# Optimization experiments

Hardware: AMD Instinct MI355X
Metric: run time of the kernel (lower is better)

The kernel has to match this reference:

```python
import jax, jax.numpy as jnp
import numpy as np

N, E, B = 30000, 100000, 1024
FXD, FXT, D, H, NOUT = 78, 954, 128, 10, 2


def setup_inputs() -> dict:
    key = jax.random.key(0)
    ks = jax.random.split(key, 24)
    rn = lambda i, shape, s=0.05: jax.random.normal(ks[i], shape, dtype=jnp.float32) * s
    z = lambda shape: jnp.zeros(shape, dtype=jnp.float32)
    batch = ((jnp.arange(N) * B) // N).astype(jnp.int32)  # sorted, every graph id present
    return {
        "x1": rn(0, (N, FXD), 1.0),
        "edge_index1": jax.random.randint(ks[1], (2, E), 0, N, dtype=jnp.int32),
        "batch1": batch,
        "x2": rn(2, (N, FXD), 1.0),
        "edge_index2": jax.random.randint(ks[3], (2, E), 0, N, dtype=jnp.int32),
        "batch2": batch,
        "cell": jax.random.uniform(ks[4], (B, FXT), dtype=jnp.float32),
        "W1": rn(5, (FXD, H * D)), "a_src1": rn(6, (1, H, D)), "a_dst1": rn(7, (1, H, D)), "b1": z((H * D,)),
        # GATConv2: 1280 -> 128, 1 head
        "W2": rn(8, (H * D, D)), "a_src2": rn(9, (1, 1, D)), "a_dst2": rn(10, (1, 1, D)), "b2": z((D,)),
        "Wg": rn(11, (D, D)), "bg": z((D,)),
        "Wr1": rn(12, (FXT, 2048)), "br1": z((2048,)),
        "Wr2": rn(13, (2048, 512)), "br2": z((512,)),
        "Wr3": rn(14, (512, 2 * D)), "br3": z((2 * D,)),
        "Wf1": rn(15, (4 * D, 1024)), "bf1": z((1024,)),
        "Wf2": rn(16, (1024, 512)), "bf2": z((512,)),
        "Wf3": rn(17, (512, 128)), "bf3": z((128,)),
        "Wo": rn(18, (128, NOUT)), "bo": z((NOUT,)),
    }


def gat_conv(x, src, dst, W, a_src, a_dst, bias, heads, ch):
    """PyG GATConv (v1), self-loops already included in src/dst. Concat heads."""
    n = x.shape[0]
    h = (x @ W).reshape(n, heads, ch)                      # [N,H,C]
    alpha_s = jnp.sum(h * a_src, axis=-1)                  # [N,H]
    alpha_d = jnp.sum(h * a_dst, axis=-1)                  # [N,H]
    e = jax.nn.leaky_relu(alpha_s[src] + alpha_d[dst], 0.2)  # [E',H]
    emax = jax.ops.segment_max(e, dst, num_segments=n)     # segment softmax over dst
    ex = jnp.exp(e - emax[dst])
    denom = jax.ops.segment_sum(ex, dst, num_segments=n)
    alpha = ex / (denom[dst] + 1e-16)                      # [E',H]
    msg = h[src] * alpha[:, :, None]                       # [E',H,C]
    out = jax.ops.segment_sum(msg, dst, num_segments=n)    # [N,H,C]
    return out.reshape(n, heads * ch) + bias


def _l2norm(x):
    return x / jnp.maximum(jnp.linalg.norm(x, axis=1, keepdims=True), 1e-12)


def reference(x1, edge_index1, batch1, x2, edge_index2, batch2, cell,
              W1, a_src1, a_dst1, b1, W2, a_src2, a_dst2, b2, Wg, bg,
              Wr1, br1, Wr2, br2, Wr3, br3, Wf1, bf1, Wf2, bf2, Wf3, bf3, Wo, bo):
    def branch(x, ei, batch):
        n = x.shape[0]
        loops = jnp.arange(n, dtype=ei.dtype)              # add_self_loops=True
        src = jnp.concatenate([ei[0], loops])
        dst = jnp.concatenate([ei[1], loops])
        h = jax.nn.elu(gat_conv(x, src, dst, W1, a_src1, a_dst1, b1, H, D))
        h = jax.nn.elu(gat_conv(h, src, dst, W2, a_src2, a_dst2, b2, 1, D))
        g = jax.ops.segment_max(h, batch, num_segments=B)  # global_max_pool
        return jax.nn.relu(g @ Wg + bg)

    v1 = branch(x1, edge_index1, batch1)
    v2 = branch(x2, edge_index2, batch2)
    c = _l2norm(cell)
    c = jax.nn.relu(c @ Wr1 + br1)
    c = jax.nn.relu(c @ Wr2 + br2)
    c = jax.nn.relu(c @ Wr3 + br3)
    xc = _l2norm(jnp.concatenate([v1, v2, c], axis=1))
    xc = jax.nn.relu(xc @ Wf1 + bf1)
    xc = jax.nn.relu(xc @ Wf2 + bf2)
    xc = jax.nn.relu(xc @ Wf3 + bf3)
    return xc @ Wo + bo
```

## Files before the change

### kernel.cpp

```cpp
#include <hip/hip_runtime.h>
#include <math.h>

typedef unsigned short ushort_t;
typedef __attribute__((ext_vector_type(8))) short short8;
typedef __attribute__((ext_vector_type(8))) unsigned short ushort8v;
typedef __attribute__((ext_vector_type(4))) float float4v;
typedef __attribute__((ext_vector_type(4))) unsigned short ushort4v;

#define MPAD 30016
#define H1STR 136

__device__ __forceinline__ float lrelu02(float v){ return v > 0.f ? v : 0.2f*v; }
__device__ __forceinline__ float elu_fast(float v){ return v > 0.f ? v : (__expf(v) - 1.f); }

__device__ __forceinline__ ushort_t f2bf(float x){
  unsigned u = __float_as_uint(x);
  return (ushort_t)((u + 0x7fffu + ((u >> 16) & 1u)) >> 16);
}
__device__ __forceinline__ float bf2f(ushort_t h){ return __uint_as_float(((unsigned)h) << 16); }

__device__ __forceinline__ unsigned encf(float f){
  unsigned u = __float_as_uint(f);
  return (u & 0x80000000u) ? ~u : (u | 0x80000000u);
}
__device__ __forceinline__ float decf(unsigned u){
  return __uint_as_float((u >> 31) ? (u & 0x7FFFFFFFu) : ~u);
}

__device__ __forceinline__ void gll16(const void* g, void* l){
  __builtin_amdgcn_global_load_lds((const __attribute__((address_space(1))) void*)g,
                                   (__attribute__((address_space(3))) void*)l, 16, 0, 0);
}

__global__ void hist2_k(const int* __restrict__ ei1, const int* __restrict__ ei2,
                        int E, int N, int* deg){
  int idx = blockIdx.x*blockDim.x + threadIdx.x;
  if (idx < 2*E){
    int br = idx / E, e = idx - br*E;
    const int* ei = br ? ei2 : ei1;
    atomicAdd(&deg[br*N + ei[E + e]], 1);
  }
}

__global__ __launch_bounds__(1024)
void scanA_k(const int* __restrict__ deg, int* __restrict__ rowptr, int* __restrict__ bsum, int n){
  int br = blockIdx.y;
  int t = threadIdx.x;
  int i = blockIdx.x*1024 + t;
  __shared__ int s[1024];
  int v = (i < n) ? (deg[br*n + i] + 1) : 0;
  s[t] = v; __syncthreads();
  for (int off = 1; off < 1024; off <<= 1){
    int x = (t >= off) ? s[t - off] : 0;
    __syncthreads();
    s[t] += x;
    __syncthreads();
  }
  if (i < n) rowptr[br*(n+1) + i] = s[t] - v;
  if (t == 1023) bsum[br*gridDim.x + blockIdx.x] = s[1023];
}

__global__ void scanB_k(int* bsum, int nb){
  int br = threadIdx.x;
  if (br < 2){
    int run = 0;
    for (int i = 0; i < nb; ++i){ int v = bsum[br*nb + i]; bsum[br*nb + i] = run; run += v; }
  }
}

__global__ __launch_bounds__(1024)
void scanC_k(const int* __restrict__ bsum, int* __restrict__ rowptr, int* __restrict__ cursor,
             int n, int nb, int total){
  int br = blockIdx.y;
  int i = blockIdx.x*1024 + threadIdx.x;
  int add = bsum[br*nb + blockIdx.x];
  if (i < n){
    int nv = rowptr[br*(n+1) + i] + add;
    rowptr[br*(n+1) + i] = nv;
    cursor[br*n + i] = nv;
  }
  if (i == 0) rowptr[br*(n+1) + n] = total;
}

__global__ void fill_csr2_k(const int* __restrict__ ei1, const int* __restrict__ ei2,
                            int E, int N, int* cursor, int* csr){
  int idx = blockIdx.x*blockDim.x + threadIdx.x;
  if (idx < 2*E){
    int br = idx / E, e = idx - br*E;
    const int* ei = br ? ei2 : ei1;
    int dst = ei[E + e];
    int pos = atomicAdd(&cursor[br*N + dst], 1);
    csr[br*(E+N) + pos] = ei[e];
  } else if (idx < 2*E + 2*N){
    int r = idx - 2*E;
    int br = r / N, i = r - br*N;
    int pos = atomicAdd(&cursor[br*N + i], 1);
    csr[br*(E+N) + pos] = i;
  }
}

__global__ void mkattn_k(const float* __restrict__ W1, const float* __restrict__ a_src1,
                         const float* __restrict__ a_dst1,
                         const float* __restrict__ W2, const float* __restrict__ a_src2,
                         const float* __restrict__ a_dst2,
                         float* As, float* Ad, float* vs, float* vd){
  int idx = blockIdx.x*blockDim.x + threadIdx.x;
  if (idx < 780){
    int f = idx / 10, h = idx % 10;
    float ss = 0.f, sd = 0.f;
    for (int c = 0; c < 128; ++c){
      float w = W1[f*1280 + h*128 + c];
      ss += w * a_src1[h*128 + c];
      sd += w * a_dst1[h*128 + c];
    }
    As[idx] = ss; Ad[idx] = sd;
  } else if (idx < 2060){
    int k = idx - 780;
    float ss = 0.f, sd = 0.f;
    for (int c = 0; c < 128; ++c){
      float w = W2[k*128 + c];
      ss += w * a_src2[c]; sd += w * a_dst2[c];
    }
    vs[k] = ss; vd[k] = sd;
  }
}

__global__ __launch_bounds__(256)
void alpha1b_k(const float* __restrict__ x1, const float* __restrict__ x2,
               const float* __restrict__ As, const float* __restrict__ Ad,
               float* as1, float* ad1, int n){
  __shared__ float sAs[780], sAd[780];
  int t = threadIdx.x;
  for (int k = t; k < 780; k += 256){ sAs[k] = As[k]; sAd[k] = Ad[k]; }
  __syncthreads();
  int idx = blockIdx.x*256 + t;
  if (idx >= 2*n) return;
  int br = idx / n, i = idx - br*n;
  const float* xr = (br ? x2 : x1) + (size_t)i*78;
  float ss[10], sd[10];
  #pragma unroll
  for (int h = 0; h < 10; ++h){ ss[h] = 0.f; sd[h] = 0.f; }
  for (int f = 0; f < 78; ++f){
    float xv = xr[f];
    #pragma unroll
    for (int h = 0; h < 10; ++h){
      ss[h] += xv * sAs[f*10 + h];
      sd[h] += xv * sAd[f*10 + h];
    }
  }
  #pragma unroll
  for (int h = 0; h < 10; ++h){
    as1[(size_t)idx*10 + h] = ss[h];
    ad1[(size_t)idx*10 + h] = sd[h];
  }
}

__global__ __launch_bounds__(64)
void gat1_agg_k(const int* __restrict__ rowptr2, const int* __restrict__ csr2,
                const float* __restrict__ x1, const float* __restrict__ x2,
                const float* __restrict__ as1b, const float* __restrict__ ad1b,
                ushort_t* __restrict__ yh, int n, int E){
  int gi = blockIdx.x;
  int br = (gi >= n) ? 1 : 0;
  int i = gi - br*n;
  int t = threadIdx.x;
  const int* rowptr = rowptr2 + (size_t)br*(n+1);
  const int* csr    = csr2 + (size_t)br*(E+n);
  const float* x    = br ? x2 : x1;
  const float* as1  = as1b + (size_t)br*n*10;
  ushort_t* yb      = yh + (size_t)br*10*MPAD*96;

  __shared__ float adi[10], rden[10], wE[10], xs[78];
  int beg = rowptr[i], end = rowptr[i+1];
  if (t < 10) adi[t] = ad1b[(size_t)gi*10 + t];
  __syncthreads();
  float den = 0.f;
  float acc[13];
  int hh[13], cc[13];
  #pragma unroll
  for (int k = 0; k < 13; ++k){
    acc[k] = 0.f;
    int j = t + 64*k;
    hh[k] = (j < 780) ? (j/78) : 0;
    cc[k] = (j < 780) ? (j%78) : 0;
  }
  for (int e = beg; e < end; ++e){
    int s = csr[e];
    if (t < 10){
      float w = __expf(lrelu02(as1[(size_t)s*10 + t] + adi[t]));
      wE[t] = w; den += w;
    }
    for (int c = t; c < 78; c += 64) xs[c] = x[(size_t)s*78 + c];
    __syncthreads();
    #pragma unroll
    for (int k = 0; k < 13; ++k){
      int j = t + 64*k;
      if (j < 780) acc[k] += wE[hh[k]] * xs[cc[k]];
    }
    __syncthreads();
  }
  if (t < 10) rden[t] = 1.f/(den + 1e-16f);
  __syncthreads();
  #pragma unroll
  for (int k = 0; k < 13; ++k){
    int j = t + 64*k;
    if (j < 780) yb[((size_t)hh[k]*MPAD + i)*96 + cc[k]] = f2bf(acc[k]*rden[hh[k]]);
  }
  for (int p = t; p < 180; p += 64){
    int h = p/18, c = 78 + p%18;
    yb[((size_t)h*MPAD + i)*96 + c] = 0;
  }
}

__global__ __launch_bounds__(256)
void branch_conv_k(const ushort_t* __restrict__ yall,
                   const ushort_t* __restrict__ W1h, const ushort_t* __restrict__ W2h,
                   const float* __restrict__ b1, const float* __restrict__ vs,
                   const float* __restrict__ vd,
                   ushort_t* __restrict__ h2all, float* __restrict__ as2all,
                   float* __restrict__ ad2all, int M){
  const int NBLK = MPAD/64;
  int br = blockIdx.x / NBLK;
  int bi = blockIdx.x - br*NBLK;
  const ushort_t* y = yall + (size_t)br*10*MPAD*96;
  ushort_t* h2 = h2all + (size_t)br*MPAD*128;
  float* as2 = as2all + (size_t)br*MPAD;
  float* ad2 = ad2all + (size_t)br*MPAD;

  __shared__ ushort_t stage[2][6144];
  __shared__ ushort_t h1t[64*H1STR];
  __shared__ float red[256];

  int tid = threadIdx.x, lane = tid & 63, wave = tid >> 6;
  int row0 = bi*64;
  int wm = (wave & 1)*32, wn = (wave >> 1)*64;
  int lr = lane & 15, quad = lane >> 4;
  int sr = lane >> 2;
  int skc = (((lane & 3) ^ ((lane >> 3) & 3)) * 8);
  int qs  = (quad ^ ((lr >> 1) & 3)) * 8;

  float4v acc2[2][4];
  #pragma unroll
  for (int i = 0; i < 2; ++i)
    #pragma unroll
    for (int j = 0; j < 4; ++j)
      acc2[i][j] = (float4v){0.f, 0.f, 0.f, 0.f};
  float rps[8], rpd[8];
  #pragma unroll
  for (int z = 0; z < 8; ++z){ rps[z] = 0.f; rpd[z] = 0.f; }

  for (int h = 0; h < 10; ++h){
    const ushort_t* gA   = y   + ((size_t)h*MPAD + row0 + wave*16 + sr)*96 + skc;
    const ushort_t* gB0h = W1h + ((size_t)(h*128 + wave*32      + sr))*96 + skc;
    const ushort_t* gB1h = W1h + ((size_t)(h*128 + wave*32 + 16 + sr))*96 + skc;
    const ushort_t* gC0h = W2h + ((size_t)(wave*32      + sr))*1280 + h*128 + skc;
    const ushort_t* gC1h = W2h + ((size_t)(wave*32 + 16 + sr))*1280 + h*128 + skc;

    auto issue1 = [&](int p, int kt){
      ushort_t* st = &stage[p][0];
      gll16(gA   + kt, st + wave*512);
      gll16(gB0h + kt, st + 2048 + wave*1024);
      gll16(gB1h + kt, st + 2048 + wave*1024 + 512);
    };
    auto issue2 = [&](int p, int kt){
      ushort_t* st = &stage[p][0];
      gll16(gC0h + kt, st + 2048 + wave*1024);
      gll16(gC1h + kt, st + 2048 + wave*1024 + 512);
    };

    __syncthreads();
    issue1(0, 0);
    float4v acc1[2][4];
    #pragma unroll
    for (int i = 0; i < 2; ++i)
      #pragma unroll
      for (int j = 0; j < 4; ++j)
        acc1[i][j] = (float4v){0.f, 0.f, 0.f, 0.f};
    int p = 0;
    #pragma unroll
    for (int it = 0; it < 3; ++it){
      __syncthreads();
      if (it < 2) issue1(p ^ 1, (it + 1)*32);
      const ushort_t* sm = &stage[p][0];
      short8 af[2], bhf[4];
      #pragma unroll
      for (int t2 = 0; t2 < 2; ++t2)
        af[t2] = *(const short8*)&sm[(wm + t2*16 + lr)*32 + qs];
      #pragma unroll
      for (int j = 0; j < 4; ++j)
        bhf[j] = *(const short8*)&sm[2048 + (wn + j*16 + lr)*32 + qs];
      #pragma unroll
      for (int i = 0; i < 2; ++i)
        #pragma unroll
        for (int j = 0; j < 4; ++j)
          acc1[i][j] = __builtin_amdgcn_mfma_f32_16x16x32_bf16(af[i], bhf[j], acc1[i][j], 0, 0, 0);
      p ^= 1;
    }

    #pragma unroll
    for (int j = 0; j < 4; ++j){
      int col = wn + j*16 + lr;
      float bv  = b1[h*128 + col];
      float vsv = vs[h*128 + col];
      float vdv = vd[h*128 + col];
      #pragma unroll
      for (int i = 0; i < 2; ++i){
        #pragma unroll
        for (int r = 0; r < 4; ++r){
          float v = elu_fast(acc1[i][j][r] + bv);
          h1t[(wm + i*16 + quad*4 + r)*H1STR + col] = f2bf(v);
          rps[i*4 + r] += v * vsv;
          rpd[i*4 + r] += v * vdv;
        }
      }
    }
    __syncthreads();

    issue2(0, 0);
    p = 0;
    #pragma unroll
    for (int it = 0; it < 4; ++it){
      __syncthreads();
      if (it < 3) issue2(p ^ 1, (it + 1)*32);
      const ushort_t* sm = &stage[p][0];
      int kt = it*32;
      short8 af[2], bhf[4];
      #pragma unroll
      for (int t2 = 0; t2 < 2; ++t2)
        af[t2] = *(const short8*)&h1t[(wm + t2*16 + lr)*H1STR + kt + quad*8];
      #pragma unroll
      for (int j = 0; j < 4; ++j)
        bhf[j] = *(const short8*)&sm[2048 + (wn + j*16 + lr)*32 + qs];
      #pragma unroll
      for (int i = 0; i < 2; ++i)
        #pragma unroll
        for (int j = 0; j < 4; ++j)
          acc2[i][j] = __builtin_amdgcn_mfma_f32_16x16x32_bf16(af[i], bhf[j], acc2[i][j], 0, 0, 0);
      p ^= 1;
    }
  }

  #pragma unroll
  for (int j = 0; j < 4; ++j){
    int col = wn + j*16 + lr;
    #pragma unroll
    for (int i = 0; i < 2; ++i){
      #pragma unroll
      for (int r = 0; r < 4; ++r){
        int row = row0 + wm + i*16 + quad*4 + r;
        if (row < M) h2[(size_t)row*128 + col] = f2bf(acc2[i][j][r]);
      }
    }
  }
  __syncthreads();
  #pragma unroll
  for (int z = 0; z < 8; ++z){
    float a = rps[z], d = rpd[z];
    #pragma unroll
    for (int mk = 1; mk <= 8; mk <<= 1){
      a += __shfl_xor(a, mk);
      d += __shfl_xor(d, mk);
    }
    if (lr == 0){
      int i = z >> 2, r = z & 3;
      int row = wm + i*16 + quad*4 + r;
      red[row*2 + (wave >> 1)] = a;
      red[128 + row*2 + (wave >> 1)] = d;
    }
  }
  __syncthreads();
  if (tid < 64){
    int grow = row0 + tid;
    if (grow < M){
      as2[grow] = red[tid*2] + red[tid*2 + 1];
      ad2[grow] = red[128 + tid*2] + red[128 + tid*2 + 1];
    }
  }
}

__global__ __launch_bounds__(64)
void gat2_agg_k(const int* __restrict__ rowptr2, const int* __restrict__ csr2,
                const ushort_t* __restrict__ h2all, const float* __restrict__ as2all,
                const float* __restrict__ ad2all, const float* __restrict__ b2,
                const int* __restrict__ batch1, const int* __restrict__ batch2,
                unsigned* __restrict__ poolKey, int n, int E, int Bg){
  int gi = blockIdx.x;
  int br = (gi >= n) ? 1 : 0;
  int i = gi - br*n;
  int t = threadIdx.x;
  const int* rowptr = rowptr2 + (size_t)br*(n+1);
  const int* csr    = csr2 + (size_t)br*(E+n);
  const ushort_t* h2 = h2all + (size_t)br*MPAD*128;
  const float* as2  = as2all + (size_t)br*MPAD;
  float adi = ad2all[(size_t)br*MPAD + i];
  int beg = rowptr[i], end = rowptr[i+1];
  float den = 0.f, a0 = 0.f, a1 = 0.f;
  for (int e = beg; e < end; ++e){
    int s = csr[e];
    float w = __expf(lrelu02(as2[s] + adi));
    den += w;
    unsigned u = *(const unsigned*)&h2[(size_t)s*128 + 2*t];
    a0 += w * bf2f((ushort_t)(u & 0xffffu));
    a1 += w * bf2f((ushort_t)(u >> 16));
  }
  float r = 1.f/(den + 1e-16f);
  float o0 = elu_fast(a0*r + b2[2*t]);
  float o1 = elu_fast(a1*r + b2[2*t + 1]);
  int g = (br ? batch2 : batch1)[i];
  unsigned* pk = poolKey + ((size_t)br*Bg + g)*128;
  atomicMax(&pk[2*t], encf(o0));
  atomicMax(&pk[2*t + 1], encf(o1));
}

__global__ void pool_decode_k(const unsigned* __restrict__ key,
                              ushort_t* __restrict__ ph, ushort_t* __restrict__ pl, int n){
  int i = blockIdx.x*blockDim.x + threadIdx.x;
  if (i < n){
    float v = decf(key[i]);
    ushort_t h = f2bf(v);
    ph[i] = h; pl[i] = f2bf(v - bf2f(h));
  }
}

__global__ __launch_bounds__(256)
void l2norm_split_k(const float* __restrict__ in, int cols, int Kp,
                    ushort_t* __restrict__ oh, ushort_t* __restrict__ ol){
  int r = blockIdx.x, t = threadIdx.x;
  __shared__ float s[256];
  __shared__ float scaleS;
  const float* rp = in + (size_t)r*cols;
  float p = 0.f;
  for (int k = t; k < cols; k += 256){ float v = rp[k]; p += v*v; }
  s[t] = p; __syncthreads();
  for (int o = 128; o > 0; o >>= 1){
    if (t < o) s[t] += s[t+o];
    __syncthreads();
  }
  if (t == 0) scaleS = 1.f / fmaxf(sqrtf(s[0]), 1e-12f);
  __syncthreads();
  float sc = scaleS;
  for (int k = t; k < Kp; k += 256){
    float v = (k < cols) ? rp[k]*sc : 0.f;
    ushort_t h = f2bf(v);
    size_t o2 = (size_t)r*Kp + k;
    oh[o2] = h; ol[o2] = f2bf(v - bf2f(h));
  }
}

__global__ __launch_bounds__(256)
void catnorm_k(const float* __restrict__ vall, const float* __restrict__ c3,
               ushort_t* __restrict__ oh, ushort_t* __restrict__ ol, int Bg){
  int r = blockIdx.x, t = threadIdx.x;
  __shared__ float s[256];
  __shared__ float scaleS;
  auto val = [&](int c)->float{
    if (c < 128) return vall[(size_t)r*128 + c];
    if (c < 256) return vall[((size_t)Bg + r)*128 + (c - 128)];
    return c3[(size_t)r*256 + (c - 256)];
  };
  float v0 = val(t), v1 = val(t + 256);
  s[t] = v0*v0 + v1*v1; __syncthreads();
  for (int o = 128; o > 0; o >>= 1){
    if (t < o) s[t] += s[t+o];
    __syncthreads();
  }
  if (t == 0) scaleS = 1.f / fmaxf(sqrtf(s[0]), 1e-12f);
  __syncthreads();
  float sc = scaleS;
  float a = v0*sc, b = v1*sc;
  ushort_t ha = f2bf(a), hb = f2bf(b);
  size_t o2 = (size_t)r*512;
  oh[o2 + t] = ha;       ol[o2 + t] = f2bf(a - bf2f(ha));
  oh[o2 + 256 + t] = hb; ol[o2 + 256 + t] = f2bf(b - bf2f(hb));
}

__global__ void act_split_k(const float* __restrict__ in, ushort_t* __restrict__ oh,
                            ushort_t* __restrict__ ol, int n){
  int i = blockIdx.x*blockDim.x + threadIdx.x;
  if (i < n){
    float v = fmaxf(in[i], 0.f);
    ushort_t h = f2bf(v);
    oh[i] = h; ol[i] = f2bf(v - bf2f(h));
  }
}

__device__ __forceinline__ void split_one(const float* __restrict__ W, int ldw, int colStride,
                                          int N, int K, int Np, int Kp,
                                          ushort_t* __restrict__ dh, ushort_t* __restrict__ dl,
                                          int idx){
  int n  = idx % Np;
  int r  = idx / Np;
  int k4 = r % (Kp >> 2);
  int b  = r / (Kp >> 2);
  size_t o = ((size_t)b*Np + n)*Kp + (size_t)k4*4;
  ushort4v hv, lv;
  #pragma unroll
  for (int kk = 0; kk < 4; ++kk){
    int k = k4*4 + kk;
    float v = (n < N && k < K) ? W[(size_t)k*ldw + (size_t)b*colStride + n] : 0.f;
    ushort_t h = f2bf(v);
    hv[kk] = h; lv[kk] = f2bf(v - bf2f(h));
  }
  *(ushort4v*)&dh[o] = hv;
  if (dl) *(ushort4v*)&dl[o] = lv;
}

struct SplitTable {
  const float *W1, *W2, *Wg, *Wr1, *Wr2, *Wr3, *Wf1, *Wf2, *Wf3, *Wo;
  ushort_t *W1h,*W2h,*Wgh,*Wgl,*Wr1h,*Wr1l,*Wr2h,*Wr2l;
  ushort_t *Wr3h,*Wr3l,*Wf1h,*Wf1l,*Wf2h,*Wf2l,*Wf3h,*Wf3l,*Woh,*Wol;
};

__global__ void split_all_k(SplitTable T){
  int idx = blockIdx.x*blockDim.x + threadIdx.x;
  if      (idx <   30720) split_one(T.W1, 1280, 128, 128,   78,  128,   96, T.W1h, nullptr, idx);
  else if (idx <   71680) split_one(T.W2,  128,   0, 128, 1280,  128, 1280, T.W2h, nullptr, idx -   30720);
  else if (idx <   75776) split_one(T.Wg,  128,   0, 128,  128,  128,  128, T.Wgh, T.Wgl, idx -   71680);
  else if (idx <  567296) split_one(T.Wr1,2048,   0,2048,  954, 2048,  960, T.Wr1h,T.Wr1l,idx -   75776);
  else if (idx <  829440) split_one(T.Wr2, 512,   0, 512, 2048,  512, 2048, T.Wr2h,T.Wr2l,idx -  567296);
  else if (idx <  862208) split_one(T.Wr3, 256,   0, 256,  512,  256,  512, T.Wr3h,T.Wr3l,idx -  829440);
  else if (idx <  993280) split_one(T.Wf1,1024,   0,1024,  512, 1024,  512, T.Wf1h,T.Wf1l,idx -  862208);
  else if (idx < 1124352) split_one(T.Wf2, 512,   0, 512, 1024,  512, 1024, T.Wf2h,T.Wf2l,idx -  993280);
  else if (idx < 1140736) split_one(T.Wf3, 128,   0, 128,  512,  128,  512, T.Wf3h,T.Wf3l,idx - 1124352);
  else if (idx < 1142784) split_one(T.Wo,    2,   0,   2,  128,   64,  128, T.Woh, T.Wol, idx - 1140736);
}

__global__ __launch_bounds__(256)
void gemm_split(const ushort_t* __restrict__ Ahp, const ushort_t* __restrict__ Alp, int lda, long long sA,
                const ushort_t* __restrict__ Bhp, const ushort_t* __restrict__ Blp, int ldb, long long sB,
                float* __restrict__ C, ushort_t* __restrict__ Ch, ushort_t* __restrict__ Cl,
                int ldc, long long sC,
                const float* __restrict__ bias, int sBias,
                int M, int Nc, int K, int act, int outMode, int kSplit, int aSplit){
  int zb = blockIdx.z;
  int b = zb / kSplit, kc = zb - b*kSplit;
  Ahp += (long long)b*sA;
  Bhp += (long long)b*sB; Blp += (long long)b*sB;
  long long cOff = (long long)b*sC;
  int Kc = K / kSplit;
  int kb = kc*Kc;
  int nIter = Kc / 32;

  __shared__ ushort_t smem[18048];

  int tid = threadIdx.x, lane = tid & 63, wave = tid >> 6;
  int row0 = blockIdx.y*64, col0 = blockIdx.x*64;
  int wm = (wave & 1)*32, wn = (wave >> 1)*32;
  int lr = lane & 15, quad = lane >> 4;
  int qs = (quad ^ ((lr >> 1) & 3)) * 8;

  int srow = wave*16 + (lane >> 2);
  int skc  = (((lane & 3) ^ ((lane >> 3) & 3)) * 8);
  const ushort_t* gAh = Ahp + (long long)(row0 + srow)*lda + skc + kb;
  const ushort_t* gAl = aSplit ? (Alp + (long long)b*sA + (long long)(row0 + srow)*lda + skc + kb) : gAh;
  const ushort_t* gBh = Bhp + (long long)(col0 + srow)*ldb + skc + kb;
  const ushort_t* gBl = Blp + (long long)(col0 + srow)*ldb + skc + kb;

  float4v acc[2][2];
  #pragma unroll
  for (int i = 0; i < 2; ++i)
    #pragma unroll
    for (int j = 0; j < 2; ++j)
      acc[i][j] = (float4v){0.f, 0.f, 0.f, 0.f};

  auto issue = [&](int p, int kt){
    ushort_t* base = &smem[p*8192 + wave*512];
    gll16(gAh + kt, base);
    if (aSplit) gll16(gAl + kt, base + 2048);
    gll16(gBh + kt, base + 4096);
    gll16(gBl + kt, base + 6144);
  };

  issue(0, 0);
  int p = 0;
  for (int it = 0; it < nIter; ++it){
    __syncthreads();
    if (it + 1 < nIter) issue(p ^ 1, (it + 1)*32);
    const ushort_t* sm = &smem[p*8192];
    short8 ah[2], al[2], bh[2], bl[2];
    #pragma unroll
    for (int t2 = 0; t2 < 2; ++t2){
      int ao = (wm + t2*16 + lr)*32 + qs;
      int bo = (wn + t2*16 + lr)*32 + qs;
      ah[t2] = *(const short8*)&sm[ao];
      if (aSplit) al[t2] = *(const short8*)&sm[2048 + ao];
      bh[t2] = *(const short8*)&sm[4096 + bo];
      bl[t2] = *(const short8*)&sm[6144 + bo];
    }
    #pragma unroll
    for (int i = 0; i < 2; ++i)
      #pragma unroll
      for (int j = 0; j < 2; ++j){
        if (aSplit)
          acc[i][j] = __builtin_amdgcn_mfma_f32_16x16x32_bf16(al[i], bh[j], acc[i][j], 0, 0, 0);
        acc[i][j] = __builtin_amdgcn_mfma_f32_16x16x32_bf16(ah[i], bl[j], acc[i][j], 0, 0, 0);
        acc[i][j] = __builtin_amdgcn_mfma_f32_16x16x32_bf16(ah[i], bh[j], acc[i][j], 0, 0, 0);
      }
    p ^= 1;
  }
  __syncthreads();

  if (outMode == 0 || outMode == 2){
    #pragma unroll
    for (int j = 0; j < 2; ++j){
      int col = col0 + wn + j*16 + lr;
      if (col >= Nc) continue;
      float bv = (bias && kc == 0) ? bias[(long long)b*sBias + col] : 0.f;
      #pragma unroll
      for (int i = 0; i < 2; ++i){
        #pragma unroll
        for (int r = 0; r < 4; ++r){
          int row = row0 + wm + i*16 + quad*4 + r;
          if (row >= M) continue;
          float v = acc[i][j][r] + bv;
          if (act == 1) v = fmaxf(v, 0.f);
          else if (act == 2) v = elu_fast(v);
          long long o = cOff + (long long)row*ldc + col;
          if (outMode == 0) C[o] = v;
          else atomicAdd(&C[o], v);
        }
      }
    }
  } else {
    float* ftile = (float*)smem;
    #pragma unroll
    for (int i = 0; i < 2; ++i)
      #pragma unroll
      for (int j = 0; j < 2; ++j)
        #pragma unroll
        for (int r = 0; r < 4; ++r)
          ftile[(wm + i*16 + quad*4 + r)*68 + wn + j*16 + lr] = acc[i][j][r];
    __syncthreads();
    int row = tid >> 2, ch = (tid & 3)*16;
    int grow = row0 + row;
    if (grow < M){
      if (col0 + 64 <= Nc){
        long long o = cOff + (long long)grow*ldc + col0 + ch;
        #pragma unroll
        for (int g = 0; g < 2; ++g){
          ushort8v hv, lv;
          #pragma unroll
          for (int c = 0; c < 8; ++c){
            int cc2 = ch + g*8 + c;
            float v = ftile[row*68 + cc2];
            if (bias) v += bias[(long long)b*sBias + col0 + cc2];
            if (act == 1) v = fmaxf(v, 0.f);
            else if (act == 2) v = elu_fast(v);
            hv[c] = f2bf(v);
            lv[c] = f2bf(v - bf2f(hv[c]));
          }
          *(ushort8v*)&Ch[o + g*8] = hv;
          *(ushort8v*)&Cl[o + g*8] = lv;
        }
      } else {
        for (int c = 0; c < 16; ++c){
          int col = col0 + ch + c;
          if (col >= Nc) break;
          float v = ftile[row*68 + ch + c];
          if (bias) v += bias[(long long)b*sBias + col];
          if (act == 1) v = fmaxf(v, 0.f);
          else if (act == 2) v = elu_fast(v);
          long long o = cOff + (long long)grow*ldc + col;
          ushort_t h = f2bf(v);
          Ch[o] = h;
          Cl[o] = f2bf(v - bf2f(h));
        }
      }
    }
  }
}

extern "C" void kernel_launch(void* const* d_in, const int* in_sizes, int n_in,
                              void* d_out, int out_size, void* d_ws, size_t ws_size,
                              hipStream_t stream){
  const float* x1     = (const float*)d_in[0];
  const int*   ei1    = (const int*)  d_in[1];
  const int*   batch1 = (const int*)  d_in[2];
  const float* x2     = (const float*)d_in[3];
  const int*   ei2    = (const int*)  d_in[4];
  const int*   batch2 = (const int*)  d_in[5];
  const float* cell   = (const float*)d_in[6];
  const float* W1     = (const float*)d_in[7];
  const float* a_src1 = (const float*)d_in[8];
  const float* a_dst1 = (const float*)d_in[9];
  const float* b1     = (const float*)d_in[10];
  const float* W2     = (const float*)d_in[11];
  const float* a_src2 = (const float*)d_in[12];
  const float* a_dst2 = (const float*)d_in[13];
  const float* b2     = (const float*)d_in[14];
  const float* Wg     = (const float*)d_in[15];
  const float* bg     = (const float*)d_in[16];
  const float* Wr1    = (const float*)d_in[17];
  const float* br1    = (const float*)d_in[18];
  const float* Wr2    = (const float*)d_in[19];
  const float* br2    = (const float*)d_in[20];
  const float* Wr3    = (const float*)d_in[21];
  const float* br3    = (const float*)d_in[22];
  const float* Wf1    = (const float*)d_in[23];
  const float* bf1    = (const float*)d_in[24];
  const float* Wf2    = (const float*)d_in[25];
  const float* bf2    = (const float*)d_in[26];
  const float* Wf3    = (const float*)d_in[27];
  const float* bf3    = (const float*)d_in[28];
  const float* Wo     = (const float*)d_in[29];
  const float* bo     = (const float*)d_in[30];
  float* out = (float*)d_out;
  (void)n_in; (void)out_size; (void)ws_size;

  const int N  = in_sizes[0] / 78;
  const int E  = in_sizes[1] / 2;
  const int Bg = in_sizes[6] / 954;

  char* wsb = (char*)d_ws;
  size_t off = 0;
  auto alloc = [&](size_t bytes)->char*{
    char* p = wsb + off; off += ((bytes + 255)/256)*256; return p;
  };

  char* Yb = alloc((size_t)2*10*MPAD*96*2);
  ushort_t* yh = (ushort_t*)Yb;
  size_t yoff = 0;
  auto yalloc = [&](size_t bytes)->char*{
    char* p = Yb + yoff; yoff += ((bytes + 255)/256)*256; return p;
  };
  ushort_t* cnh  = (ushort_t*)yalloc((size_t)Bg*960*2);
  ushort_t* cnl  = (ushort_t*)yalloc((size_t)Bg*960*2);
  ushort_t* c1h  = (ushort_t*)yalloc((size_t)Bg*2048*2);
  ushort_t* c1l  = (ushort_t*)yalloc((size_t)Bg*2048*2);
  ushort_t* c2h  = (ushort_t*)yalloc((size_t)Bg*512*2);
  ushort_t* c2l  = (ushort_t*)yalloc((size_t)Bg*512*2);
  float*    c3   = (float*)   yalloc((size_t)Bg*256*4);
  ushort_t* xcnh = (ushort_t*)yalloc((size_t)Bg*512*2);
  ushort_t* xcnl = (ushort_t*)yalloc((size_t)Bg*512*2);
  ushort_t* t1h  = (ushort_t*)yalloc((size_t)Bg*1024*2);
  ushort_t* t1l  = (ushort_t*)yalloc((size_t)Bg*1024*2);
  ushort_t* t2h  = (ushort_t*)yalloc((size_t)Bg*512*2);
  ushort_t* t2l  = (ushort_t*)yalloc((size_t)Bg*512*2);
  ushort_t* t3h  = (ushort_t*)yalloc((size_t)Bg*128*2);
  ushort_t* t3l  = (ushort_t*)yalloc((size_t)Bg*128*2);
  ushort_t* pooledh = (ushort_t*)yalloc((size_t)2*Bg*128*2);
  ushort_t* pooledl = (ushort_t*)yalloc((size_t)2*Bg*128*2);
  float*    vall    = (float*)   yalloc((size_t)2*Bg*128*4);

  size_t zElems = (size_t)Bg*512 + (size_t)Bg*512 + (size_t)Bg*128 + (size_t)2*Bg*128
                + (size_t)2*N;
  float* zbase = (float*)alloc(zElems*4);
  float* c2f = zbase;
  float* t2f = c2f + (size_t)Bg*512;
  float* t3f = t2f + (size_t)Bg*512;
  unsigned* poolKey = (unsigned*)(t3f + (size_t)Bg*128);
  int* deg2 = (int*)(poolKey + (size_t)2*Bg*128);

  ushort_t* h2 = (ushort_t*)alloc((size_t)2*MPAD*128*2);
  float* as2 = (float*)alloc((size_t)2*MPAD*4);
  float* ad2 = (float*)alloc((size_t)2*MPAD*4);

  ushort_t* W1th = (ushort_t*)alloc((size_t)10*128*96*2);
  ushort_t* W2th = (ushort_t*)alloc((size_t)128*1280*2);
  ushort_t* Wgth = (ushort_t*)alloc((size_t)128*128*2);
  ushort_t* Wgtl = (ushort_t*)alloc((size_t)128*128*2);
  ushort_t* Wr1th= (ushort_t*)alloc((size_t)2048*960*2);
  ushort_t* Wr1tl= (ushort_t*)alloc((size_t)2048*960*2);
  ushort_t* Wr2th= (ushort_t*)alloc((size_t)512*2048*2);
  ushort_t* Wr2tl= (ushort_t*)alloc((size_t)512*2048*2);
  ushort_t* Wr3th= (ushort_t*)alloc((size_t)256*512*2);
  ushort_t* Wr3tl= (ushort_t*)alloc((size_t)256*512*2);
  ushort_t* Wf1th= (ushort_t*)alloc((size_t)1024*512*2);
  ushort_t* Wf1tl= (ushort_t*)alloc((size_t)1024*512*2);
  ushort_t* Wf2th= (ushort_t*)alloc((size_t)512*1024*2);
  ushort_t* Wf2tl= (ushort_t*)alloc((size_t)512*1024*2);
  ushort_t* Wf3th= (ushort_t*)alloc((size_t)128*512*2);
  ushort_t* Wf3tl= (ushort_t*)alloc((size_t)128*512*2);
  ushort_t* Woth = (ushort_t*)alloc((size_t)64*128*2);
  ushort_t* Wotl = (ushort_t*)alloc((size_t)64*128*2);

  float* as1b = (float*)alloc((size_t)2*N*10*4);
  float* ad1b = (float*)alloc((size_t)2*N*10*4);
  float* AsB  = (float*)alloc(780*4);
  float* AdB  = (float*)alloc(780*4);
  float* vs   = (float*)alloc(1280*4);
  float* vd   = (float*)alloc(1280*4);
  int* rowptr2 = (int*)alloc((size_t)2*(N+1)*4);
  int* cursor2 = (int*)alloc((size_t)2*N*4);
  int* csr2    = (int*)alloc((size_t)2*(E+N)*4);
  int* bsum    = (int*)alloc((size_t)2*64*4);

  auto gemm = [&](const ushort_t* Ah_, const ushort_t* Al_, int lda, long long sA_,
                  const ushort_t* Bh_, const ushort_t* Bl_, int ldb, long long sB_,
                  float* C_, ushort_t* Ch_, ushort_t* Cl_, int ldc, long long sC_,
                  const float* bias_, int sBias_, int M_, int N_, int K_, int batch_,
                  int act_, int mode_, int kSplit_, int aSplit_){
    dim3 grid((N_ + 63)/64, (M_ + 63)/64, batch_*kSplit_);
    gemm_split<<<grid, 256, 0, stream>>>(Ah_, Al_, lda, sA_, Bh_, Bl_, ldb, sB_,
                                         C_, Ch_, Cl_, ldc, sC_, bias_, sBias_,
                                         M_, N_, K_, act_, mode_, kSplit_, aSplit_);
  };

  hipMemsetAsync(zbase, 0, zElems*4, stream);
  SplitTable T;
  T.W1 = W1; T.W2 = W2; T.Wg = Wg; T.Wr1 = Wr1; T.Wr2 = Wr2; T.Wr3 = Wr3;
  T.Wf1 = Wf1; T.Wf2 = Wf2; T.Wf3 = Wf3; T.Wo = Wo;
  T.W1h = W1th; T.W2h = W2th; T.Wgh = Wgth; T.Wgl = Wgtl;
  T.Wr1h = Wr1th; T.Wr1l = Wr1tl; T.Wr2h = Wr2th; T.Wr2l = Wr2tl;
  T.Wr3h = Wr3th; T.Wr3l = Wr3tl; T.Wf1h = Wf1th; T.Wf1l = Wf1tl;
  T.Wf2h = Wf2th; T.Wf2l = Wf2tl; T.Wf3h = Wf3th; T.Wf3l = Wf3tl;
  T.Woh = Woth; T.Wol = Wotl;
  split_all_k<<<(1142784 + 255)/256, 256, 0, stream>>>(T);
  mkattn_k<<<(2060 + 255)/256, 256, 0, stream>>>(W1, a_src1, a_dst1, W2, a_src2, a_dst2,
                                                 AsB, AdB, vs, vd);
  alpha1b_k<<<((2*N) + 255)/256, 256, 0, stream>>>(x1, x2, AsB, AdB, as1b, ad1b, N);

  const int NB = (N + 1023)/1024;
  hist2_k<<<((2*E) + 255)/256, 256, 0, stream>>>(ei1, ei2, E, N, deg2);
  scanA_k<<<dim3(NB, 2), 1024, 0, stream>>>(deg2, rowptr2, bsum, N);
  scanB_k<<<1, 64, 0, stream>>>(bsum, NB);
  scanC_k<<<dim3(NB, 2), 1024, 0, stream>>>(bsum, rowptr2, cursor2, N, NB, E + N);
  fill_csr2_k<<<((2*E + 2*N) + 255)/256, 256, 0, stream>>>(ei1, ei2, E, N, cursor2, csr2);

  gat1_agg_k<<<2*N, 64, 0, stream>>>(rowptr2, csr2, x1, x2, as1b, ad1b, yh, N, E);
  branch_conv_k<<<2*(MPAD/64), 256, 0, stream>>>(yh, W1th, W2th,
                                                 b1, vs, vd, h2, as2, ad2, N);
  gat2_agg_k<<<2*N, 64, 0, stream>>>(rowptr2, csr2, h2, as2, ad2, b2,
                                     batch1, batch2, poolKey, N, E, Bg);
  pool_decode_k<<<((2*Bg*128) + 255)/256, 256, 0, stream>>>(poolKey, pooledh, pooledl, 2*Bg*128);
  gemm(pooledh, pooledl, 128, 0, Wgth, Wgtl, 128, 0,
       vall, nullptr, nullptr, 128, 0, bg, 0, 2*Bg, 128, 128, 1, 1, 0, 1, 1);

  l2norm_split_k<<<Bg, 256, 0, stream>>>(cell, 954, 960, cnh, cnl);
  gemm(cnh, cnl, 960, 0, Wr1th, Wr1tl, 960, 0, nullptr, c1h, c1l, 2048, 0,
       br1, 0, Bg, 2048, 960, 1, 1, 1, 1, 1);
  gemm(c1h, c1l, 2048, 0, Wr2th, Wr2tl, 2048, 0, c2f, nullptr, nullptr, 512, 0,
       br2, 0, Bg, 512, 2048, 1, 0, 2, 4, 1);
  act_split_k<<<((Bg*512) + 255)/256, 256, 0, stream>>>(c2f, c2h, c2l, Bg*512);
  gemm(c2h, c2l, 512, 0, Wr3th, Wr3tl, 512, 0, c3, nullptr, nullptr, 256, 0,
       br3, 0, Bg, 256, 512, 1, 1, 0, 1, 1);

  catnorm_k<<<Bg, 256, 0, stream>>>(vall, c3, xcnh, xcnl, Bg);
  gemm(xcnh, xcnl, 512, 0, Wf1th, Wf1tl, 512, 0, nullptr, t1h, t1l, 1024, 0,
       bf1, 0, Bg, 1024, 512, 1, 1, 1, 1, 1);
  gemm(t1h, t1l, 1024, 0, Wf2th, Wf2tl, 1024, 0, t2f, nullptr, nullptr, 512, 0,
       bf2, 0, Bg, 512, 1024, 1, 0, 2, 4, 1);
  act_split_k<<<((Bg*512) + 255)/256, 256, 0, stream>>>(t2f, t2h, t2l, Bg*512);
  gemm(t2h, t2l, 512, 0, Wf3th, Wf3tl, 512, 0, t3f, nullptr, nullptr, 128, 0,
       bf3, 0, Bg, 128, 512, 1, 0, 2, 4, 1);
  act_split_k<<<((Bg*128) + 255)/256, 256, 0, stream>>>(t3f, t3h, t3l, Bg*128);
  gemm(t3h, t3l, 128, 0, Woth, Wotl, 128, 0, out, nullptr, nullptr, 2, 0,
       bo, 0, Bg, 2, 128, 1, 0, 0, 1, 1);
}
```

Before: 564.0 us.

## Double row tile in fused GAT conv GEMM and process two edges per aggregation step

The fused branch conv kernel now handles 128 rows per block instead of 64, with each wave computing a 64x64 tile. This reuses every W1/W2 tile load across twice as many rows and halves the block count, at the cost of more LDS and accumulator registers, which may reduce occupancy. MPAD is padded to a multiple of 128. Both GAT aggregation kernels now unroll the edge loop by two, so each pair of edges shares one pair of barriers and the loads have more memory-level parallelism.

```diff
diff --git a/kernel.cpp b/kernel.cpp
--- a/kernel.cpp
+++ b/kernel.cpp
@@ -7,7 +7,7 @@
 typedef __attribute__((ext_vector_type(4))) float float4v;
 typedef __attribute__((ext_vector_type(4))) unsigned short ushort4v;
 
-#define MPAD 30016
+#define MPAD 30080
 #define H1STR 136
 
 __device__ __forceinline__ float lrelu02(float v){ return v > 0.f ? v : 0.2f*v; }
@@ -170,9 +170,10 @@
   const float* as1  = as1b + (size_t)br*n*10;
   ushort_t* yb      = yh + (size_t)br*10*MPAD*96;
 
-  __shared__ float adi[10], rden[10], wE[10], xs[78];
+  __shared__ float adi[10], rden[10], wE[2][10], xs0[78], xs1[78];
   int beg = rowptr[i], end = rowptr[i+1];
   if (t < 10) adi[t] = ad1b[(size_t)gi*10 + t];
+  for (int c = t; c < 78; c += 64) xs1[c] = 0.f;
   __syncthreads();
   float den = 0.f;
   float acc[13];
@@ -184,18 +185,22 @@
     hh[k] = (j < 780) ? (j/78) : 0;
     cc[k] = (j < 780) ? (j%78) : 0;
   }
-  for (int e = beg; e < end; ++e){
-    int s = csr[e];
+  for (int e = beg; e < end; e += 2){
+    int s0 = csr[e];
+    int s1 = (e + 1 < end) ? csr[e + 1] : -1;
     if (t < 10){
-      float w = __expf(lrelu02(as1[(size_t)s*10 + t] + adi[t]));
-      wE[t] = w; den += w;
-    }
-    for (int c = t; c < 78; c += 64) xs[c] = x[(size_t)s*78 + c];
+      float w0 = __expf(lrelu02(as1[(size_t)s0*10 + t] + adi[t]));
+      float w1 = (s1 >= 0) ? __expf(lrelu02(as1[(size_t)s1*10 + t] + adi[t])) : 0.f;
+      wE[0][t] = w0; wE[1][t] = w1; den += w0 + w1;
+    }
+    for (int c = t; c < 78; c += 64) xs0[c] = x[(size_t)s0*78 + c];
+    if (s1 >= 0)
+      for (int c = t; c < 78; c += 64) xs1[c] = x[(size_t)s1*78 + c];
     __syncthreads();
     #pragma unroll
     for (int k = 0; k < 13; ++k){
       int j = t + 64*k;
-      if (j < 780) acc[k] += wE[hh[k]] * xs[cc[k]];
+      if (j < 780) acc[k] += wE[0][hh[k]]*xs0[cc[k]] + wE[1][hh[k]]*xs1[cc[k]];
     }
     __syncthreads();
   }
@@ -219,7 +224,7 @@
                    const float* __restrict__ vd,
                    ushort_t* __restrict__ h2all, float* __restrict__ as2all,
                    float* __restrict__ ad2all, int M){
-  const int NBLK = MPAD/64;
+  const int NBLK = MPAD/128;
   int br = blockIdx.x / NBLK;
   int bi = blockIdx.x - br*NBLK;
   const ushort_t* y = yall + (size_t)br*10*MPAD*96;
@@ -227,52 +232,54 @@
   float* as2 = as2all + (size_t)br*MPAD;
   float* ad2 = ad2all + (size_t)br*MPAD;
 
-  __shared__ ushort_t stage[2][6144];
-  __shared__ ushort_t h1t[64*H1STR];
-  __shared__ float red[256];
+  __shared__ ushort_t stage[2][8192];
+  __shared__ ushort_t h1t[128*H1STR];
+  __shared__ float red[512];
 
   int tid = threadIdx.x, lane = tid & 63, wave = tid >> 6;
-  int row0 = bi*64;
-  int wm = (wave & 1)*32, wn = (wave >> 1)*64;
+  int row0 = bi*128;
+  int wm = (wave & 1)*64, wn = (wave >> 1)*64;
   int lr = lane & 15, quad = lane >> 4;
   int sr = lane >> 2;
   int skc = (((lane & 3) ^ ((lane >> 3) & 3)) * 8);
   int qs  = (quad ^ ((lr >> 1) & 3)) * 8;
 
-  float4v acc2[2][4];
-  #pragma unroll
-  for (int i = 0; i < 2; ++i)
+  float4v acc2[4][4];
+  #pragma unroll
+  for (int i = 0; i < 4; ++i)
     #pragma unroll
     for (int j = 0; j < 4; ++j)
       acc2[i][j] = (float4v){0.f, 0.f, 0.f, 0.f};
-  float rps[8], rpd[8];
-  #pragma unroll
-  for (int z = 0; z < 8; ++z){ rps[z] = 0.f; rpd[z] = 0.f; }
+  float rps[16], rpd[16];
+  #pragma unroll
+  for (int z = 0; z < 16; ++z){ rps[z] = 0.f; rpd[z] = 0.f; }
 
   for (int h = 0; h < 10; ++h){
-    const ushort_t* gA   = y   + ((size_t)h*MPAD + row0 + wave*16 + sr)*96 + skc;
-    const ushort_t* gB0h = W1h + ((size_t)(h*128 + wave*32      + sr))*96 + skc;
-    const ushort_t* gB1h = W1h + ((size_t)(h*128 + wave*32 + 16 + sr))*96 + skc;
-    const ushort_t* gC0h = W2h + ((size_t)(wave*32      + sr))*1280 + h*128 + skc;
-    const ushort_t* gC1h = W2h + ((size_t)(wave*32 + 16 + sr))*1280 + h*128 + skc;
+    const ushort_t* gA0 = y   + ((size_t)h*MPAD + row0 + wave*32 + sr)*96 + skc;
+    const ushort_t* gA1 = gA0 + (size_t)16*96;
+    const ushort_t* gB0 = W1h + ((size_t)(h*128 + wave*32 + sr))*96 + skc;
+    const ushort_t* gB1 = gB0 + (size_t)16*96;
+    const ushort_t* gC0 = W2h + ((size_t)(wave*32 + sr))*1280 + h*128 + skc;
+    const ushort_t* gC1 = gC0 + (size_t)16*1280;
 
     auto issue1 = [&](int p, int kt){
       ushort_t* st = &stage[p][0];
-      gll16(gA   + kt, st + wave*512);
-      gll16(gB0h + kt, st + 2048 + wave*1024);
-      gll16(gB1h + kt, st + 2048 + wave*1024 + 512);
+      gll16(gA0 + kt, st + wave*1024);
+      gll16(gA1 + kt, st + wave*1024 + 512);
+      gll16(gB0 + kt, st + 4096 + wave*1024);
+      gll16(gB1 + kt, st + 4096 + wave*1024 + 512);
     };
     auto issue2 = [&](int p, int kt){
       ushort_t* st = &stage[p][0];
-      gll16(gC0h + kt, st + 2048 + wave*1024);
-      gll16(gC1h + kt, st + 2048 + wave*1024 + 512);
+      gll16(gC0 + kt, st + 4096 + wave*1024);
+      gll16(gC1 + kt, st + 4096 + wave*1024 + 512);
     };
 
     __syncthreads();
     issue1(0, 0);
-    float4v acc1[2][4];
-    #pragma unroll
-    for (int i = 0; i < 2; ++i)
+    float4v acc1[4][4];
+    #pragma unroll
+    for (int i = 0; i < 4; ++i)
       #pragma unroll
       for (int j = 0; j < 4; ++j)
         acc1[i][j] = (float4v){0.f, 0.f, 0.f, 0.f};
@@ -282,18 +289,18 @@
       __syncthreads();
       if (it < 2) issue1(p ^ 1, (it + 1)*32);
       const ushort_t* sm = &stage[p][0];
-      short8 af[2], bhf[4];
-      #pragma unroll
-      for (int t2 = 0; t2 < 2; ++t2)
+      short8 af[4], bf[4];
+      #pragma unroll
+      for (int t2 = 0; t2 < 4; ++t2)
         af[t2] = *(const short8*)&sm[(wm + t2*16 + lr)*32 + qs];
       #pragma unroll
       for (int j = 0; j < 4; ++j)
-        bhf[j] = *(const short8*)&sm[2048 + (wn + j*16 + lr)*32 + qs];
-      #pragma unroll
-      for (int i = 0; i < 2; ++i)
+        bf[j] = *(const short8*)&sm[4096 + (wn + j*16 + lr)*32 + qs];
+      #pragma unroll
+      for (int i = 0; i < 4; ++i)
         #pragma unroll
         for (int j = 0; j < 4; ++j)
-          acc1[i][j] = __builtin_amdgcn_mfma_f32_16x16x32_bf16(af[i], bhf[j], acc1[i][j], 0, 0, 0);
+          acc1[i][j] = __builtin_amdgcn_mfma_f32_16x16x32_bf16(af[i], bf[j], acc1[i][j], 0, 0, 0);
       p ^= 1;
     }
 
@@ -304,7 +311,7 @@
       float vsv = vs[h*128 + col];
       float vdv = vd[h*128 + col];
       #pragma unroll
-      for (int i = 0; i < 2; ++i){
+      for (int i = 0; i < 4; ++i){
         #pragma unroll
         for (int r = 0; r < 4; ++r){
           float v = elu_fast(acc1[i][j][r] + bv);
@@ -324,18 +331,18 @@
       if (it < 3) issue2(p ^ 1, (it + 1)*32);
       const ushort_t* sm = &stage[p][0];
       int kt = it*32;
-      short8 af[2], bhf[4];
-      #pragma unroll
-      for (int t2 = 0; t2 < 2; ++t2)
+      short8 af[4], bf[4];
+      #pragma unroll
+      for (int t2 = 0; t2 < 4; ++t2)
         af[t2] = *(const short8*)&h1t[(wm + t2*16 + lr)*H1STR + kt + quad*8];
       #pragma unroll
       for (int j = 0; j < 4; ++j)
-        bhf[j] = *(const short8*)&sm[2048 + (wn + j*16 + lr)*32 + qs];
-      #pragma unroll
-      for (int i = 0; i < 2; ++i)
+        bf[j] = *(const short8*)&sm[4096 + (wn + j*16 + lr)*32 + qs];
+      #pragma unroll
+      for (int i = 0; i < 4; ++i)
         #pragma unroll
         for (int j = 0; j < 4; ++j)
-          acc2[i][j] = __builtin_amdgcn_mfma_f32_16x16x32_bf16(af[i], bhf[j], acc2[i][j], 0, 0, 0);
+          acc2[i][j] = __builtin_amdgcn_mfma_f32_16x16x32_bf16(af[i], bf[j], acc2[i][j], 0, 0, 0);
       p ^= 1;
     }
   }
@@ -344,7 +351,7 @@
   for (int j = 0; j < 4; ++j){
     int col = wn + j*16 + lr;
     #pragma unroll
-    for (int i = 0; i < 2; ++i){
+    for (int i = 0; i < 4; ++i){
       #pragma unroll
       for (int r = 0; r < 4; ++r){
         int row = row0 + wm + i*16 + quad*4 + r;
@@ -354,7 +361,7 @@
   }
   __syncthreads();
   #pragma unroll
-  for (int z = 0; z < 8; ++z){
+  for (int z = 0; z < 16; ++z){
     float a = rps[z], d = rpd[z];
     #pragma unroll
     for (int mk = 1; mk <= 8; mk <<= 1){
@@ -363,17 +370,17 @@
     }
     if (lr == 0){
       int i = z >> 2, r = z & 3;
-      int row = wm + i*16 + quad*4 + r;
-      red[row*2 + (wave >> 1)] = a;
-      red[128 + row*2 + (wave >> 1)] = d;
+      int rowl = wm + i*16 + quad*4 + r;
+      red[rowl*2 + (wave >> 1)] = a;
+      red[256 + rowl*2 + (wave >> 1)] = d;
     }
   }
   __syncthreads();
-  if (tid < 64){
+  if (tid < 128){
     int grow = row0 + tid;
     if (grow < M){
       as2[grow] = red[tid*2] + red[tid*2 + 1];
-      ad2[grow] = red[128 + tid*2] + red[128 + tid*2 + 1];
+      ad2[grow] = red[256 + tid*2] + red[256 + tid*2 + 1];
     }
   }
 }
@@ -395,13 +402,17 @@
   float adi = ad2all[(size_t)br*MPAD + i];
   int beg = rowptr[i], end = rowptr[i+1];
   float den = 0.f, a0 = 0.f, a1 = 0.f;
-  for (int e = beg; e < end; ++e){
-    int s = csr[e];
-    float w = __expf(lrelu02(as2[s] + adi));
-    den += w;
-    unsigned u = *(const unsigned*)&h2[(size_t)s*128 + 2*t];
-    a0 += w * bf2f((ushort_t)(u & 0xffffu));
-    a1 += w * bf2f((ushort_t)(u >> 16));
+  for (int e = beg; e < end; e += 2){
+    int s0 = csr[e];
+    int valid1 = (e + 1 < end);
+    int s1 = valid1 ? csr[e + 1] : s0;
+    float w0 = __expf(lrelu02(as2[s0] + adi));
+    float w1 = valid1 ? __expf(lrelu02(as2[s1] + adi)) : 0.f;
+    den += w0 + w1;
+    unsigned u0 = *(const unsigned*)&h2[(size_t)s0*128 + 2*t];
+    unsigned u1 = *(const unsigned*)&h2[(size_t)s1*128 + 2*t];
+    a0 += w0 * bf2f((ushort_t)(u0 & 0xffffu)) + w1 * bf2f((ushort_t)(u1 & 0xffffu));
+    a1 += w0 * bf2f((ushort_t)(u0 >> 16))     + w1 * bf2f((ushort_t)(u1 >> 16));
   }
   float r = 1.f/(den + 1e-16f);
   float o0 = elu_fast(a0*r + b2[2*t]);
@@ -818,8 +829,8 @@
   fill_csr2_k<<<((2*E + 2*N) + 255)/256, 256, 0, stream>>>(ei1, ei2, E, N, cursor2, csr2);
 
   gat1_agg_k<<<2*N, 64, 0, stream>>>(rowptr2, csr2, x1, x2, as1b, ad1b, yh, N, E);
-  branch_conv_k<<<2*(MPAD/64), 256, 0, stream>>>(yh, W1th, W2th,
-                                                 b1, vs, vd, h2, as2, ad2, N);
+  branch_conv_k<<<2*(MPAD/128), 256, 0, stream>>>(yh, W1th, W2th,
+                                                  b1, vs, vd, h2, as2, ad2, N);
   gat2_agg_k<<<2*N, 64, 0, stream>>>(rowptr2, csr2, h2, as2, ad2, b2,
                                      batch1, batch2, poolKey, N, E, Bg);
   pool_decode_k<<<((2*Bg*128) + 255)/256, 256, 0, stream>>>(poolKey, pooledh, pooledl, 2*Bg*128);
```

Measured after the change: 593.7 us. 5.3% more time.
